# Performance work log

Hardware: AMD Instinct MI355X
Metric: run time of the kernel (lower is better)

Reference implementation:

```python
import jax, jax.numpy as jnp
import numpy as np

NF = 32      # feature channels
DG = 4       # deformable groups
K = 9        # 3x3 kernel taps


def _conv(x, w, b, stride=1):
    # x: [B,C,H,W], w: [O,I,3,3] (pad=1)
    y = jax.lax.conv_general_dilated(x, w, (stride, stride), ((1, 1), (1, 1)),
                                     dimension_numbers=('NCHW', 'OIHW', 'NCHW'))
    return y + b[None, :, None, None]


def _lrelu(x):
    return jnp.where(x >= 0, x, 0.1 * x)


def _up2(x):
    # bilinear, align_corners=False (half-pixel centers, matches torch F.interpolate)
    B, C, H, W = x.shape
    return jax.image.resize(x, (B, C, 2 * H, 2 * W), method='bilinear')


def _deform_conv(x, om, w, b):
    # Modulated deformable conv (DCNv2), stride=1, pad=1, dilation=1, 3x3.
    # x: [B,C,H,W]; om: [B,3*DG*K,H,W] = (offset_y | offset_x | mask) blocks.
    B, C, H, W = x.shape
    Cg = C // DG
    o1, o2, m = jnp.split(om, 3, axis=1)
    off_y = o1.reshape(B, DG, K, H, W)
    off_x = o2.reshape(B, DG, K, H, W)
    mask = jax.nn.sigmoid(m).reshape(B, DG, K, H, W)
    k = jnp.arange(K)
    dy = (k // 3 - 1).astype(x.dtype)            # kernel tap y displacement
    dx = (k % 3 - 1).astype(x.dtype)
    # sampling positions [B,DG,K,H,W]
    py = off_y + jnp.arange(H, dtype=x.dtype)[:, None] + dy[:, None, None]
    px = off_x + jnp.arange(W, dtype=x.dtype)[None, :] + dx[:, None, None]
    y0 = jnp.floor(py)
    x0 = jnp.floor(px)
    wy1 = py - y0
    wx1 = px - x0
    y0i = y0.astype(jnp.int32)
    x0i = x0.astype(jnp.int32)
    imgf = x.reshape(B, DG, Cg, H * W)

    def corner(yi, xi, wt):
        valid = (yi >= 0) & (yi < H) & (xi >= 0) & (xi < W)
        yc = jnp.clip(yi, 0, H - 1)
        xc = jnp.clip(xi, 0, W - 1)
        idx = (yc * W + xc).reshape(B, DG, 1, K * H * W)
        v = jnp.take_along_axis(imgf, idx, axis=3).reshape(B, DG, Cg, K, H, W)
        return v * (wt * valid)[:, :, None]

    samp = (corner(y0i, x0i, (1 - wy1) * (1 - wx1))
            + corner(y0i, x0i + 1, (1 - wy1) * wx1)
            + corner(y0i + 1, x0i, wy1 * (1 - wx1))
            + corner(y0i + 1, x0i + 1, wy1 * wx1))
    samp = samp * mask[:, :, None]                       # [B,DG,Cg,K,H,W]
    out = jnp.einsum('bgckhw,ogck->bohw', samp, w.reshape(w.shape[0], DG, Cg, K))
    return out + b[None, :, None, None]


_PARAM_SHAPES = [
    ('w1_1', (32, 64, 3, 3)), ('b1_1', (32,)),
    ('w2_1', (32, 32, 3, 3)), ('b2_1', (32,)),
    ('w3_1', (32, 32, 3, 3)), ('b3_1', (32,)),
    ('w4_1', (32, 32, 3, 3)), ('b4_1', (32,)),
    ('w6_1', (32, 32, 3, 3)), ('b6_1', (32,)),
    ('w7_1', (32, 32, 3, 3)), ('b7_1', (32,)),
    ('w1_2', (32, 64, 3, 3)), ('b1_2', (32,)),
    ('w2_2', (32, 32, 3, 3)), ('b2_2', (32,)),
    ('w3_2', (32, 64, 3, 3)), ('b3_2', (32,)),
    ('w4_2', (32, 32, 3, 3)), ('b4_2', (32,)),
    ('w_om', (108, 32, 3, 3)), ('b_om', (108,)),   # DCN_sep conv_offset_mask: 3*DG*K=108
    ('w_dcn', (32, 32, 3, 3)), ('b_dcn', (32,)),
]


def setup_inputs() -> dict:
    key = jax.random.key(0)
    ks = jax.random.split(key, len(_PARAM_SHAPES) + 2)
    B, H, W = 4, 192, 192
    d = {
        'fea1': jax.random.normal(ks[0], (B, NF, H, W), jnp.float32),
        'fea2': jax.random.normal(ks[1], (B, NF, H, W), jnp.float32),
    }
    for i, (name, shp) in enumerate(_PARAM_SHAPES):
        d[name] = jax.random.normal(ks[i + 2], shp, jnp.float32) * 0.05
    return d


def reference(fea1, fea2, w1_1, b1_1, w2_1, b2_1, w3_1, b3_1, w4_1, b4_1,
              w6_1, b6_1, w7_1, b7_1, w1_2, b1_2, w2_2, b2_2, w3_2, b3_2,
              w4_2, b4_2, w_om, b_om, w_dcn, b_dcn):
    off = _lrelu(_conv(jnp.concatenate([fea1, fea2], 1), w1_1, b1_1))
    off1 = _lrelu(_conv(off, w2_1, b2_1))
    off2 = _lrelu(_conv(off1, w3_1, b3_1, 2))   # H/2
    off2 = _lrelu(_conv(off2, w4_1, b4_1))
    off3 = _lrelu(_conv(off2, w6_1, b6_1, 2))   # H/4
    off3 = _lrelu(_conv(off3, w7_1, b7_1))
    up = _up2(off3)                              # back to H/2
    off = _lrelu(_conv(jnp.concatenate([up, off2], 1), w1_2, b1_2))
    off = _lrelu(_conv(off, w2_2, b2_2))
    up = _up2(off)                               # back to H
    off = _lrelu(_conv(jnp.concatenate([up, off1], 1), w3_2, b3_2))
    base_offset = _conv(off, w4_2, b4_2)
    om = _conv(base_offset, w_om, b_om)          # DCN_sep offset/mask head
    return _deform_conv(fea2, om, w_dcn, b_dcn)
```

## Files before the change

kernel.cpp:

```cpp
#include <hip/hip_runtime.h>
#include <math.h>


#define BDIM 256

typedef __attribute__((ext_vector_type(8))) short short8v;
typedef __attribute__((ext_vector_type(4))) float f32x4;

__device__ __forceinline__ unsigned short f2bf(float f) {
    unsigned u = __builtin_bit_cast(unsigned, f);
    u = (u + 0x7FFF + ((u >> 16) & 1)) >> 16;
    return (unsigned short)u;
}
__device__ __forceinline__ float bf2f(unsigned short h) {
    unsigned u = ((unsigned)h) << 16;
    return __builtin_bit_cast(float, u);
}

template<int NPASS, bool LRELU, int YS>
__global__ __launch_bounds__(BDIM, 2)
void convr_k(const short* __restrict__ in0, const short* __restrict__ in1,
             const short* __restrict__ wf,
             const float* __restrict__ bias,
             short* __restrict__ out, int H, int W)
{
    const int lane = threadIdx.x & 63;
    const int wid  = blockIdx.x * 4 + (threadIdx.x >> 6);
    const int segs = W >> 4;
    const int strips = (H / YS) * segs;
    const int b = wid / strips;
    int r = wid - b * strips;
    const int ys = r / segs;
    const int y0 = ys * YS;
    const int x0 = (r - ys * segs) * 16;
    const int lp = lane & 15;
    const int g  = lane >> 4;

    int colOff[3]; bool colOk[3];
#pragma unroll
    for (int tx = 0; tx < 3; ++tx) {
        const int ix = x0 + lp + tx - 1;
        colOk[tx] = (unsigned)ix < (unsigned)W;
        colOff[tx] = min(max(ix, 0), W - 1) * 32 + g * 8;
    }

    const size_t inPlane = (size_t)H * W * 32;
    const short8v zero = {};
    const short* inp0 = in0 + (size_t)b * inPlane;
    const short* inp1 = (NPASS > 1) ? in1 + (size_t)b * inPlane : nullptr;

    short8v awc[(NPASS == 1) ? 18 : 1];
    if constexpr (NPASS == 1) {
#pragma unroll
        for (int t = 0; t < 9; ++t)
#pragma unroll
            for (int h = 0; h < 2; ++h)
                awc[t * 2 + h] = *(const short8v*)(
                    wf + (((size_t)t * 2 + h) * 64 + lane) * 8);
    }

    short8v win[NPASS][3][3];

#define LOADROW(SLOT, IY) do {                                                \
        const int iy_ = (IY);                                                 \
        const bool rok_ = (unsigned)iy_ < (unsigned)H;                        \
        const int ro_ = min(max(iy_, 0), H - 1) * W;                          \
        _Pragma("unroll")                                                     \
        for (int tx = 0; tx < 3; ++tx) {                                      \
            short8v v_ = *(const short8v*)(inp0 + (size_t)ro_ * 32 + colOff[tx]); \
            win[0][SLOT][tx] = (rok_ & colOk[tx]) ? v_ : zero;                \
            if constexpr (NPASS > 1) {                                        \
                short8v w_ = *(const short8v*)(inp1 + (size_t)ro_ * 32 + colOff[tx]); \
                win[1][SLOT][tx] = (rok_ & colOk[tx]) ? w_ : zero;            \
            }                                                                 \
        }                                                                     \
    } while (0)

    LOADROW(0, y0 - 1);
    LOADROW(1, y0);

#pragma unroll
    for (int s = 0; s < YS; ++s) {
        LOADROW((s + 2) % 3, y0 + s + 1);

        f32x4 a0 = (f32x4){0.f, 0.f, 0.f, 0.f};
        f32x4 a1 = (f32x4){0.f, 0.f, 0.f, 0.f};
#pragma unroll
        for (int p = 0; p < NPASS; ++p) {
#pragma unroll
            for (int ty = 0; ty < 3; ++ty) {
#pragma unroll
                for (int tx = 0; tx < 3; ++tx) {
                    const int t = ty * 3 + tx;
                    const short8v bv = win[p][(s + ty) % 3][tx];
                    short8v av0, av1;
                    if constexpr (NPASS == 1) {
                        av0 = awc[t * 2 + 0];
                        av1 = awc[t * 2 + 1];
                    } else {
                        av0 = *(const short8v*)(
                            wf + ((((size_t)p * 9 + t) * 2 + 0) * 64 + lane) * 8);
                        av1 = *(const short8v*)(
                            wf + ((((size_t)p * 9 + t) * 2 + 1) * 64 + lane) * 8);
                    }
                    a0 = __builtin_amdgcn_mfma_f32_16x16x32_bf16(av0, bv, a0, 0, 0, 0);
                    a1 = __builtin_amdgcn_mfma_f32_16x16x32_bf16(av1, bv, a1, 0, 0, 0);
                }
            }
        }

        short* op = out + (((size_t)b * H + (y0 + s)) * W + x0 + lp) * 32;
        ushort4 st0, st1;
#pragma unroll
        for (int j = 0; j < 4; ++j) {
            float v0 = a0[j] + bias[g * 4 + j];
            float v1 = a1[j] + bias[16 + g * 4 + j];
            if (LRELU) {
                v0 = (v0 >= 0.f) ? v0 : 0.1f * v0;
                v1 = (v1 >= 0.f) ? v1 : 0.1f * v1;
            }
            ((unsigned short*)&st0)[j] = f2bf(v0);
            ((unsigned short*)&st1)[j] = f2bf(v1);
        }
        *(ushort4*)(op + g * 4) = st0;
        *(ushort4*)(op + 16 + g * 4) = st1;
    }
#undef LOADROW
}

template<int NPASS, int NHALF, int STRIDE, bool LRELU>
__global__ __launch_bounds__(BDIM, 4)
void convm_k(const short* __restrict__ in0, const short* __restrict__ in1,
             const short* __restrict__ wf,
             const float* __restrict__ bias,
             short* __restrict__ out,
             int Hin, int Win, int Hout, int Wout, int OCS)
{
    const int lane = threadIdx.x & 63;
    const int wid  = blockIdx.x * 4 + (threadIdx.x >> 6);
    const int segs = Wout >> 4;
    const int b  = wid / (Hout * segs);
    int r = wid - b * (Hout * segs);
    const int oy = r / segs;
    const int x0 = (r - oy * segs) * 16;
    const int lp = lane & 15;
    const int g  = lane >> 4;

    int rowOff[3]; bool rowOk[3];
#pragma unroll
    for (int ty = 0; ty < 3; ++ty) {
        const int iy = oy * STRIDE + ty - 1;
        rowOk[ty] = (unsigned)iy < (unsigned)Hin;
        rowOff[ty] = min(max(iy, 0), Hin - 1) * Win;
    }
    int colOff[3]; bool colOk[3];
#pragma unroll
    for (int tx = 0; tx < 3; ++tx) {
        const int ix = (x0 + lp) * STRIDE + tx - 1;
        colOk[tx] = (unsigned)ix < (unsigned)Win;
        colOff[tx] = min(max(ix, 0), Win - 1) * 32 + g * 8;
    }

    f32x4 acc[NHALF];
#pragma unroll
    for (int h = 0; h < NHALF; ++h) acc[h] = (f32x4){0.f, 0.f, 0.f, 0.f};

    const size_t inPlane = (size_t)Hin * Win * 32;
    const short8v zero = {};

#pragma unroll
    for (int pass = 0; pass < NPASS; ++pass) {
        const short* inp = (pass == 0 ? in0 : in1) + (size_t)b * inPlane;

        short8v bv[9];
#pragma unroll
        for (int t = 0; t < 9; ++t) {
            const int ty = t / 3, tx = t % 3;
            short8v v = *(const short8v*)(inp + (size_t)rowOff[ty] * 32 + colOff[tx]);
            bv[t] = (rowOk[ty] & colOk[tx]) ? v : zero;
        }
#pragma unroll
        for (int t = 0; t < 9; ++t) {
#pragma unroll
            for (int h = 0; h < NHALF; ++h) {
                short8v av = *(const short8v*)(
                    wf + ((((size_t)pass * 9 + t) * NHALF + h) * 64 + lane) * 8);
                acc[h] = __builtin_amdgcn_mfma_f32_16x16x32_bf16(av, bv[t], acc[h], 0, 0, 0);
            }
        }
    }

    short* op = out + (((size_t)b * Hout + oy) * Wout + x0 + lp) * OCS;
#pragma unroll
    for (int h = 0; h < NHALF; ++h) {
        const int co0 = h * 16 + g * 4;
        ushort4 st;
#pragma unroll
        for (int j = 0; j < 4; ++j) {
            float v = acc[h][j] + bias[co0 + j];
            if (LRELU) v = (v >= 0.f) ? v : 0.1f * v;
            ((unsigned short*)&st)[j] = f2bf(v);
        }
        *(ushort4*)(op + co0) = st;
    }
}

struct WPArgs {
    const float* src[11];
    int off[11];
    int npass[11], nhalf[11], O[11];
};

__global__ __launch_bounds__(BDIM)
void wprep_k(WPArgs a, short* __restrict__ wbase)
{
    const int z = blockIdx.z;
    const int n = a.npass[z] * 9 * a.nhalf[z] * 512;
    const int idx = blockIdx.x * BDIM + threadIdx.x;
    if (idx >= n) return;
    const int j = idx & 7;
    const int l = (idx >> 3) & 63;
    int r = idx >> 9;
    const int h = r % a.nhalf[z]; r /= a.nhalf[z];
    const int t = r % 9;
    const int pass = r / 9;
    const int I = a.npass[z] * 32;
    const int cout = h * 16 + (l & 15);
    const int cin  = pass * 32 + (l >> 4) * 8 + j;
    float v = (cout < a.O[z]) ? a.src[z][((size_t)cout * I + cin) * 9 + t] : 0.f;
    wbase[a.off[z] + idx] = (short)f2bf(v);
}

__global__ __launch_bounds__(BDIM)
void wdp_k(const float* __restrict__ w, short* __restrict__ dst)
{
    const int idx = blockIdx.x * BDIM + threadIdx.x;
    if (idx >= 9 * 2 * 64 * 8) return;
    const int j = idx & 7;
    const int l = (idx >> 3) & 63;
    const int h = (idx >> 9) & 1;
    const int k = idx >> 10;
    const int cout = h * 16 + (l & 15);
    const int cin  = (l >> 4) * 8 + j;
    dst[idx] = (short)f2bf(w[((size_t)cout * 32 + cin) * 9 + k]);
}

__global__ __launch_bounds__(BDIM)
void cvtnhwc_k(const float* __restrict__ s0, const float* __restrict__ s1,
               short* __restrict__ d0, short* __restrict__ d1, int H, int W)
{
    const float* s = blockIdx.z ? s1 : s0;
    short* d = blockIdx.z ? d1 : d0;
    const int idx = blockIdx.x * BDIM + threadIdx.x;
    if (idx >= 4 * 32 * H * W) return;
    const int c = idx & 31;
    int t = idx >> 5;
    const int x = t % W; t /= W;
    const int y = t % H;
    const int b = t / H;
    d[idx] = (short)f2bf(s[(((size_t)b * 32 + c) * H + y) * W + x]);
}

__global__ __launch_bounds__(BDIM)
void up2b_k(const short* __restrict__ in, short* __restrict__ out,
            int Hin, int Win)
{
    const int Hout = 2 * Hin, Wout = 2 * Win;
    const int idx = blockIdx.x * BDIM + threadIdx.x;
    if (idx >= 4 * Hout * Wout * 4) return;
    const int cg = idx & 3;
    int t = idx >> 2;
    const int x = t % Wout; t /= Wout;
    const int y = t % Hout;
    const int b = t / Hout;

    const float sy = (y + 0.5f) * 0.5f - 0.5f;
    const float sx = (x + 0.5f) * 0.5f - 0.5f;
    const float y0f = floorf(sy), x0f = floorf(sx);
    const float wy = sy - y0f, wx = sx - x0f;
    const int y0 = (int)y0f, x0 = (int)x0f;
    const int y0c = min(max(y0, 0), Hin - 1);
    const int y1c = min(max(y0 + 1, 0), Hin - 1);
    const int x0c = min(max(x0, 0), Win - 1);
    const int x1c = min(max(x0 + 1, 0), Win - 1);

    const short* base = in + (size_t)b * Hin * Win * 32 + cg * 8;
    short8v v00 = *(const short8v*)(base + ((size_t)y0c * Win + x0c) * 32);
    short8v v01 = *(const short8v*)(base + ((size_t)y0c * Win + x1c) * 32);
    short8v v10 = *(const short8v*)(base + ((size_t)y1c * Win + x0c) * 32);
    short8v v11 = *(const short8v*)(base + ((size_t)y1c * Win + x1c) * 32);

    short8v o;
#pragma unroll
    for (int j = 0; j < 8; ++j) {
        float f = (1.f - wy) * ((1.f - wx) * bf2f((unsigned short)v00[j]) +
                                wx * bf2f((unsigned short)v01[j]))
                + wy * ((1.f - wx) * bf2f((unsigned short)v10[j]) +
                        wx * bf2f((unsigned short)v11[j]));
        o[j] = (short)f2bf(f);
    }
    short* op = out + (size_t)b * Hout * Wout * 32 + ((size_t)y * Wout + x) * 32 + cg * 8;
    *(short8v*)op = o;
}

__global__ __launch_bounds__(BDIM, 4)
void dcnm_k(const short* __restrict__ xb,
            const short* __restrict__ bo,
            const short* __restrict__ wfo,
            const float* __restrict__ obias,
            const short* __restrict__ wfd,
            const float* __restrict__ bias,
            float* __restrict__ out, int H, int W)
{
    __shared__ unsigned short omld[4][16][112];

    const int lane = threadIdx.x & 63;
    const int wv   = threadIdx.x >> 6;
    const int wid  = blockIdx.x * 4 + wv;
    const int segs = W >> 4;
    const int b = wid / (H * segs);
    int r = wid - b * (H * segs);
    const int y = r / segs;
    const int x0 = (r - y * segs) * 16;
    const int lp = lane & 15;
    const int g  = lane >> 4;
    const int x  = x0 + lp;
    const size_t plane = (size_t)H * W;
    const short8v zero = {};

    {
        int rowOff[3]; bool rowOk[3];
#pragma unroll
        for (int ty = 0; ty < 3; ++ty) {
            const int iy = y + ty - 1;
            rowOk[ty] = (unsigned)iy < (unsigned)H;
            rowOff[ty] = min(max(iy, 0), H - 1) * W;
        }
        int colOff[3]; bool colOk[3];
#pragma unroll
        for (int tx = 0; tx < 3; ++tx) {
            const int ix = x + tx - 1;
            colOk[tx] = (unsigned)ix < (unsigned)W;
            colOff[tx] = min(max(ix, 0), W - 1) * 32 + g * 8;
        }
        const short* inp = bo + (size_t)b * plane * 32;
        short8v bv[9];
#pragma unroll
        for (int t = 0; t < 9; ++t) {
            const int ty = t / 3, tx = t % 3;
            short8v v = *(const short8v*)(inp + (size_t)rowOff[ty] * 32 + colOff[tx]);
            bv[t] = (rowOk[ty] & colOk[tx]) ? v : zero;
        }
        f32x4 acc[7];
#pragma unroll
        for (int h = 0; h < 7; ++h) acc[h] = (f32x4){0.f, 0.f, 0.f, 0.f};
#pragma unroll
        for (int t = 0; t < 9; ++t) {
#pragma unroll
            for (int h = 0; h < 7; ++h) {
                short8v av = *(const short8v*)(wfo + (((size_t)t * 7 + h) * 64 + lane) * 8);
                acc[h] = __builtin_amdgcn_mfma_f32_16x16x32_bf16(av, bv[t], acc[h], 0, 0, 0);
            }
        }
#pragma unroll
        for (int h = 0; h < 7; ++h) {
            const int co0 = h * 16 + g * 4;
            ushort4 st;
#pragma unroll
            for (int j = 0; j < 4; ++j)
                ((unsigned short*)&st)[j] = f2bf(acc[h][j] + obias[min(co0 + j, 107)]);
            *(ushort4*)&omld[wv][lp][co0] = st;
        }
    }

    f32x4 p0 = (f32x4){0.f, 0.f, 0.f, 0.f};
    f32x4 p1 = (f32x4){0.f, 0.f, 0.f, 0.f};
    const short* xbb = xb + (size_t)b * plane * 32 + g * 8;

#pragma unroll
    for (int k = 0; k < 9; ++k) {
        const float offy = bf2f(omld[wv][lp][g * 9 + k]);
        const float offx = bf2f(omld[wv][lp][36 + g * 9 + k]);
        const float ml   = bf2f(omld[wv][lp][72 + g * 9 + k]);
        const float m = 1.f / (1.f + __expf(-ml));

        const float py = offy + (float)y + (float)(k / 3 - 1);
        const float px = offx + (float)x + (float)(k % 3 - 1);
        const float y0f = floorf(py), x0f = floorf(px);
        const int y0 = (int)y0f, x0i = (int)x0f;
        const float wy1 = py - y0f, wx1 = px - x0f;
        const float wy0 = 1.f - wy1, wx0 = 1.f - wx1;

        const bool y0ok = (unsigned)y0 < (unsigned)H;
        const bool y1ok = (unsigned)(y0 + 1) < (unsigned)H;
        const bool x0ok = (unsigned)x0i < (unsigned)W;
        const bool x1ok = (unsigned)(x0i + 1) < (unsigned)W;
        const int y0c = min(max(y0, 0), H - 1);
        const int y1c = min(max(y0 + 1, 0), H - 1);
        const int x0c = min(max(x0i, 0), W - 1);
        const int x1c = min(max(x0i + 1, 0), W - 1);

        const float w00 = wy0 * wx0 * ((y0ok && x0ok) ? 1.f : 0.f) * m;
        const float w01 = wy0 * wx1 * ((y0ok && x1ok) ? 1.f : 0.f) * m;
        const float w10 = wy1 * wx0 * ((y1ok && x0ok) ? 1.f : 0.f) * m;
        const float w11 = wy1 * wx1 * ((y1ok && x1ok) ? 1.f : 0.f) * m;

        short8v v00 = *(const short8v*)(xbb + ((size_t)y0c * W + x0c) * 32);
        short8v v01 = *(const short8v*)(xbb + ((size_t)y0c * W + x1c) * 32);
        short8v v10 = *(const short8v*)(xbb + ((size_t)y1c * W + x0c) * 32);
        short8v v11 = *(const short8v*)(xbb + ((size_t)y1c * W + x1c) * 32);

        short8v bv;
#pragma unroll
        for (int j = 0; j < 8; ++j) {
            float s = w00 * bf2f((unsigned short)v00[j])
                    + w01 * bf2f((unsigned short)v01[j])
                    + w10 * bf2f((unsigned short)v10[j])
                    + w11 * bf2f((unsigned short)v11[j]);
            bv[j] = (short)f2bf(s);
        }

        short8v a0 = *(const short8v*)(wfd + (((size_t)k * 2 + 0) * 64 + lane) * 8);
        short8v a1 = *(const short8v*)(wfd + (((size_t)k * 2 + 1) * 64 + lane) * 8);
        p0 = __builtin_amdgcn_mfma_f32_16x16x32_bf16(a0, bv, p0, 0, 0, 0);
        p1 = __builtin_amdgcn_mfma_f32_16x16x32_bf16(a1, bv, p1, 0, 0, 0);
    }

    float* op = out + (size_t)b * 32 * plane + (size_t)y * W + x;
#pragma unroll
    for (int j = 0; j < 4; ++j) {
        const int co0 = g * 4 + j;
        const int co1 = 16 + g * 4 + j;
        op[(size_t)co0 * plane] = p0[j] + bias[co0];
        op[(size_t)co1 * plane] = p1[j] + bias[co1];
    }
}


extern "C" void kernel_launch(void* const* d_in, const int* in_sizes, int n_in,
                              void* d_out, int out_size, void* d_ws, size_t ws_size,
                              hipStream_t stream)
{
    const float* fea1  = (const float*)d_in[0];
    const float* fea2  = (const float*)d_in[1];
    const float* w1_1  = (const float*)d_in[2];  const float* b1_1 = (const float*)d_in[3];
    const float* w2_1  = (const float*)d_in[4];  const float* b2_1 = (const float*)d_in[5];
    const float* w3_1  = (const float*)d_in[6];  const float* b3_1 = (const float*)d_in[7];
    const float* w4_1  = (const float*)d_in[8];  const float* b4_1 = (const float*)d_in[9];
    const float* w6_1  = (const float*)d_in[10]; const float* b6_1 = (const float*)d_in[11];
    const float* w7_1  = (const float*)d_in[12]; const float* b7_1 = (const float*)d_in[13];
    const float* w1_2  = (const float*)d_in[14]; const float* b1_2 = (const float*)d_in[15];
    const float* w2_2  = (const float*)d_in[16]; const float* b2_2 = (const float*)d_in[17];
    const float* w3_2  = (const float*)d_in[18]; const float* b3_2 = (const float*)d_in[19];
    const float* w4_2  = (const float*)d_in[20]; const float* b4_2 = (const float*)d_in[21];
    const float* w_om  = (const float*)d_in[22]; const float* b_om = (const float*)d_in[23];
    const float* w_dcn = (const float*)d_in[24]; const float* b_dcn= (const float*)d_in[25];

    const int H = 192, W = 192;
    char* ws = (char*)d_ws;

    short* fea1b = (short*)(ws + 0);
    short* fea2b = (short*)(ws + 9437184);
    short* bufA  = (short*)(ws + 18874368);
    short* bufB  = (short*)(ws + 28311552);
    short* bufC  = (short*)(ws + 0);
    short* bufD  = (short*)(ws + 2359296);
    short* bufE  = (short*)(ws + 4718592);
    short* bufF  = (short*)(ws + 5308416);
    short* bufG  = (short*)(ws + 5898240);
    short* bufH  = (short*)(ws + 0);
    short* bufI  = (short*)(ws + 4718592);
    short* bufJ  = (short*)(ws + 37748736);
    short* bufK  = (short*)(ws + 18874368);
    short* bufL  = (short*)(ws + 0);
    short* wfrag = (short*)(ws + 70778880);
    short* wfdcn = (short*)(ws + 71083008);

    const int WOFF[11] = {0, 18432, 27648, 36864, 46080, 55296,
                          64512, 82944, 92160, 110592, 119808};

    dim3 blk(BDIM, 1, 1);

    {
        WPArgs a;
        const float* srcs[11] = {w1_1, w2_1, w3_1, w4_1, w6_1, w7_1,
                                 w1_2, w2_2, w3_2, w4_2, w_om};
        const int NP[11] = {2,1,1,1,1,1,2,1,2,1,1};
        const int NH[11] = {2,2,2,2,2,2,2,2,2,2,7};
        const int Os[11] = {32,32,32,32,32,32,32,32,32,32,108};
        for (int i = 0; i < 11; ++i) {
            a.src[i] = srcs[i]; a.off[i] = WOFF[i];
            a.npass[i] = NP[i]; a.nhalf[i] = NH[i]; a.O[i] = Os[i];
        }
        wprep_k<<<dim3(126, 1, 11), blk, 0, stream>>>(a, wfrag);
        cvtnhwc_k<<<dim3(18432, 1, 2), blk, 0, stream>>>(fea1, fea2, fea1b, fea2b, H, W);
        wdp_k<<<dim3(36), blk, 0, stream>>>(w_dcn, wfdcn);
    }

    convr_k<2,true,4><<<dim3(576), blk, 0, stream>>>(
        fea1b, fea2b, wfrag + WOFF[0], b1_1, bufA, 192, 192);
    convr_k<1,true,4><<<dim3(576), blk, 0, stream>>>(
        bufA, nullptr, wfrag + WOFF[1], b2_1, bufB, 192, 192);
    convm_k<1,2,2,true><<<dim3(576), blk, 0, stream>>>(
        bufB, nullptr, wfrag + WOFF[2], b3_1, bufC, 192,192,96,96, 32);
    convm_k<1,2,1,true><<<dim3(576), blk, 0, stream>>>(
        bufC, nullptr, wfrag + WOFF[3], b4_1, bufD, 96,96,96,96, 32);
    convm_k<1,2,2,true><<<dim3(144), blk, 0, stream>>>(
        bufD, nullptr, wfrag + WOFF[4], b6_1, bufE, 96,96,48,48, 32);
    convm_k<1,2,1,true><<<dim3(144), blk, 0, stream>>>(
        bufE, nullptr, wfrag + WOFF[5], b7_1, bufF, 48,48,48,48, 32);
    up2b_k<<<dim3(576), blk, 0, stream>>>(bufF, bufG, 48, 48);
    convm_k<2,2,1,true><<<dim3(576), blk, 0, stream>>>(
        bufG, bufD, wfrag + WOFF[6], b1_2, bufH, 96,96,96,96, 32);
    convm_k<1,2,1,true><<<dim3(576), blk, 0, stream>>>(
        bufH, nullptr, wfrag + WOFF[7], b2_2, bufI, 96,96,96,96, 32);
    up2b_k<<<dim3(2304), blk, 0, stream>>>(bufI, bufJ, 96, 96);
    convr_k<2,true,4><<<dim3(576), blk, 0, stream>>>(
        bufJ, bufB, wfrag + WOFF[8], b3_2, bufK, 192, 192);
    convr_k<1,false,4><<<dim3(576), blk, 0, stream>>>(
        bufK, nullptr, wfrag + WOFF[9], b4_2, bufL, 192, 192);
    dcnm_k<<<dim3(2304), blk, 0, stream>>>(
        fea2b, bufL, wfrag + WOFF[10], b_om, wfdcn, b_dcn, (float*)d_out, H, W);
}
```

Measured before the change: 313.3 us.

## Batch DCN gather loads, shrink conv row strips, retune launch bounds

The deformable-conv kernel now computes all bilinear weights and gather indices first, then issues the twelve corner loads for three taps together before the blend-and-MFMA step. This exposes more memory-level parallelism for the gathers. The LDS row for the offset/mask tile is padded from 112 to 116, presumably to cut bank conflicts. The full-resolution convs switch from 4-row to 2-row strips with twice as many blocks, and launch-bound occupancy hints change (convr 2→3, dcnm 4→3). The trade-offs are higher register pressure from the batched loads and less vertical reuse in the smaller conv strips.

```diff
diff --git a/kernel.cpp b/kernel.cpp
--- a/kernel.cpp
+++ b/kernel.cpp
@@ -18,7 +18,7 @@
 }
 
 template<int NPASS, bool LRELU, int YS>
-__global__ __launch_bounds__(BDIM, 2)
+__global__ __launch_bounds__(BDIM, 3)
 void convr_k(const short* __restrict__ in0, const short* __restrict__ in1,
              const short* __restrict__ wf,
              const float* __restrict__ bias,
@@ -303,7 +303,7 @@
     *(short8v*)op = o;
 }
 
-__global__ __launch_bounds__(BDIM, 4)
+__global__ __launch_bounds__(BDIM, 3)
 void dcnm_k(const short* __restrict__ xb,
             const short* __restrict__ bo,
             const short* __restrict__ wfo,
@@ -312,7 +312,7 @@
             const float* __restrict__ bias,
             float* __restrict__ out, int H, int W)
 {
-    __shared__ unsigned short omld[4][16][112];
+    __shared__ unsigned short omld[4][16][116];
 
     const int lane = threadIdx.x & 63;
     const int wv   = threadIdx.x >> 6;
@@ -373,10 +373,8 @@
         }
     }
 
-    f32x4 p0 = (f32x4){0.f, 0.f, 0.f, 0.f};
-    f32x4 p1 = (f32x4){0.f, 0.f, 0.f, 0.f};
-    const short* xbb = xb + (size_t)b * plane * 32 + g * 8;
-
+    float wts[9][4];
+    int   ia[9][4];
 #pragma unroll
     for (int k = 0; k < 9; ++k) {
         const float offy = bf2f(omld[wv][lp][g * 9 + k]);
@@ -400,30 +398,47 @@
         const int x0c = min(max(x0i, 0), W - 1);
         const int x1c = min(max(x0i + 1, 0), W - 1);
 
-        const float w00 = wy0 * wx0 * ((y0ok && x0ok) ? 1.f : 0.f) * m;
-        const float w01 = wy0 * wx1 * ((y0ok && x1ok) ? 1.f : 0.f) * m;
-        const float w10 = wy1 * wx0 * ((y1ok && x0ok) ? 1.f : 0.f) * m;
-        const float w11 = wy1 * wx1 * ((y1ok && x1ok) ? 1.f : 0.f) * m;
-
-        short8v v00 = *(const short8v*)(xbb + ((size_t)y0c * W + x0c) * 32);
-        short8v v01 = *(const short8v*)(xbb + ((size_t)y0c * W + x1c) * 32);
-        short8v v10 = *(const short8v*)(xbb + ((size_t)y1c * W + x0c) * 32);
-        short8v v11 = *(const short8v*)(xbb + ((size_t)y1c * W + x1c) * 32);
-
-        short8v bv;
-#pragma unroll
-        for (int j = 0; j < 8; ++j) {
-            float s = w00 * bf2f((unsigned short)v00[j])
-                    + w01 * bf2f((unsigned short)v01[j])
-                    + w10 * bf2f((unsigned short)v10[j])
-                    + w11 * bf2f((unsigned short)v11[j]);
-            bv[j] = (short)f2bf(s);
-        }
-
-        short8v a0 = *(const short8v*)(wfd + (((size_t)k * 2 + 0) * 64 + lane) * 8);
-        short8v a1 = *(const short8v*)(wfd + (((size_t)k * 2 + 1) * 64 + lane) * 8);
-        p0 = __builtin_amdgcn_mfma_f32_16x16x32_bf16(a0, bv, p0, 0, 0, 0);
-        p1 = __builtin_amdgcn_mfma_f32_16x16x32_bf16(a1, bv, p1, 0, 0, 0);
+        wts[k][0] = wy0 * wx0 * ((y0ok && x0ok) ? 1.f : 0.f) * m;
+        wts[k][1] = wy0 * wx1 * ((y0ok && x1ok) ? 1.f : 0.f) * m;
+        wts[k][2] = wy1 * wx0 * ((y1ok && x0ok) ? 1.f : 0.f) * m;
+        wts[k][3] = wy1 * wx1 * ((y1ok && x1ok) ? 1.f : 0.f) * m;
+        ia[k][0] = y0c * W + x0c;
+        ia[k][1] = y0c * W + x1c;
+        ia[k][2] = y1c * W + x0c;
+        ia[k][3] = y1c * W + x1c;
+    }
+
+    f32x4 p0 = (f32x4){0.f, 0.f, 0.f, 0.f};
+    f32x4 p1 = (f32x4){0.f, 0.f, 0.f, 0.f};
+    const short* xbb = xb + (size_t)b * plane * 32 + g * 8;
+
+#pragma unroll
+    for (int gi = 0; gi < 3; ++gi) {
+        short8v cd[12];
+#pragma unroll
+        for (int t = 0; t < 3; ++t) {
+            const int k = gi * 3 + t;
+#pragma unroll
+            for (int c = 0; c < 4; ++c)
+                cd[t * 4 + c] = *(const short8v*)(xbb + (size_t)ia[k][c] * 32);
+        }
+#pragma unroll
+        for (int t = 0; t < 3; ++t) {
+            const int k = gi * 3 + t;
+            short8v bv;
+#pragma unroll
+            for (int j = 0; j < 8; ++j) {
+                float s = wts[k][0] * bf2f((unsigned short)cd[t * 4 + 0][j])
+                        + wts[k][1] * bf2f((unsigned short)cd[t * 4 + 1][j])
+                        + wts[k][2] * bf2f((unsigned short)cd[t * 4 + 2][j])
+                        + wts[k][3] * bf2f((unsigned short)cd[t * 4 + 3][j]);
+                bv[j] = (short)f2bf(s);
+            }
+            short8v a0 = *(const short8v*)(wfd + (((size_t)k * 2 + 0) * 64 + lane) * 8);
+            short8v a1 = *(const short8v*)(wfd + (((size_t)k * 2 + 1) * 64 + lane) * 8);
+            p0 = __builtin_amdgcn_mfma_f32_16x16x32_bf16(a0, bv, p0, 0, 0, 0);
+            p1 = __builtin_amdgcn_mfma_f32_16x16x32_bf16(a1, bv, p1, 0, 0, 0);
+        }
     }
 
     float* op = out + (size_t)b * 32 * plane + (size_t)y * W + x;
@@ -497,9 +512,9 @@
         wdp_k<<<dim3(36), blk, 0, stream>>>(w_dcn, wfdcn);
     }
 
-    convr_k<2,true,4><<<dim3(576), blk, 0, stream>>>(
+    convr_k<2,true,2><<<dim3(1152), blk, 0, stream>>>(
         fea1b, fea2b, wfrag + WOFF[0], b1_1, bufA, 192, 192);
-    convr_k<1,true,4><<<dim3(576), blk, 0, stream>>>(
+    convr_k<1,true,2><<<dim3(1152), blk, 0, stream>>>(
         bufA, nullptr, wfrag + WOFF[1], b2_1, bufB, 192, 192);
     convm_k<1,2,2,true><<<dim3(576), blk, 0, stream>>>(
         bufB, nullptr, wfrag + WOFF[2], b3_1, bufC, 192,192,96,96, 32);
@@ -515,9 +530,9 @@
     convm_k<1,2,1,true><<<dim3(576), blk, 0, stream>>>(
         bufH, nullptr, wfrag + WOFF[7], b2_2, bufI, 96,96,96,96, 32);
     up2b_k<<<dim3(2304), blk, 0, stream>>>(bufI, bufJ, 96, 96);
-    convr_k<2,true,4><<<dim3(576), blk, 0, stream>>>(
+    convr_k<2,true,2><<<dim3(1152), blk, 0, stream>>>(
         bufJ, bufB, wfrag + WOFF[8], b3_2, bufK, 192, 192);
-    convr_k<1,false,4><<<dim3(576), blk, 0, stream>>>(
+    convr_k<1,false,2><<<dim3(1152), blk, 0, stream>>>(
         bufK, nullptr, wfrag + WOFF[9], b4_2, bufL, 192, 192);
     dcnm_k<<<dim3(2304), blk, 0, stream>>>(
         fea2b, bufL, wfrag + WOFF[10], b_om, wfdcn, b_dcn, (float*)d_out, H, W);
```

New measurement: 311.2 us. No clear change (-0.7%).

## Split convr output channels across waves and shrink row strips for parallelism

Applied to the files above, without the earlier changes.

Each full-resolution conv wave now computes only one 16-channel half of the output (chosen by wave parity), with strips shortened from four rows to two, so the grid grows fourfold. This lowers per-wave register use, which allows higher launch-bound occupancy, and gives more waves to hide latency. The cost is that each input window is loaded twice, once per half, and rows are reloaded more often with shorter strips. The DCN shared-memory row is also padded from 112 to 116 to reduce bank conflicts.

```diff
diff --git a/kernel.cpp b/kernel.cpp
--- a/kernel.cpp
+++ b/kernel.cpp
@@ -18,7 +18,7 @@
 }
 
 template<int NPASS, bool LRELU, int YS>
-__global__ __launch_bounds__(BDIM, 2)
+__global__ __launch_bounds__(BDIM, NPASS == 1 ? 4 : 3)
 void convr_k(const short* __restrict__ in0, const short* __restrict__ in1,
              const short* __restrict__ wf,
              const float* __restrict__ bias,
@@ -26,10 +26,12 @@
 {
     const int lane = threadIdx.x & 63;
     const int wid  = blockIdx.x * 4 + (threadIdx.x >> 6);
+    const int hh   = wid & 1;
+    const int sw   = wid >> 1;
     const int segs = W >> 4;
     const int strips = (H / YS) * segs;
-    const int b = wid / strips;
-    int r = wid - b * strips;
+    const int b = sw / strips;
+    int r = sw - b * strips;
     const int ys = r / segs;
     const int y0 = ys * YS;
     const int x0 = (r - ys * segs) * 16;
@@ -49,15 +51,10 @@
     const short* inp0 = in0 + (size_t)b * inPlane;
     const short* inp1 = (NPASS > 1) ? in1 + (size_t)b * inPlane : nullptr;
 
-    short8v awc[(NPASS == 1) ? 18 : 1];
-    if constexpr (NPASS == 1) {
-#pragma unroll
-        for (int t = 0; t < 9; ++t)
-#pragma unroll
-            for (int h = 0; h < 2; ++h)
-                awc[t * 2 + h] = *(const short8v*)(
-                    wf + (((size_t)t * 2 + h) * 64 + lane) * 8);
-    }
+    short8v awc[9];
+#pragma unroll
+    for (int t = 0; t < 9; ++t)
+        awc[t] = *(const short8v*)(wf + (((size_t)t * 2 + hh) * 64 + lane) * 8);
 
     short8v win[NPASS][3][3];
 
@@ -84,7 +81,6 @@
         LOADROW((s + 2) % 3, y0 + s + 1);
 
         f32x4 a0 = (f32x4){0.f, 0.f, 0.f, 0.f};
-        f32x4 a1 = (f32x4){0.f, 0.f, 0.f, 0.f};
 #pragma unroll
         for (int p = 0; p < NPASS; ++p) {
 #pragma unroll
@@ -93,37 +89,27 @@
                 for (int tx = 0; tx < 3; ++tx) {
                     const int t = ty * 3 + tx;
                     const short8v bv = win[p][(s + ty) % 3][tx];
-                    short8v av0, av1;
-                    if constexpr (NPASS == 1) {
-                        av0 = awc[t * 2 + 0];
-                        av1 = awc[t * 2 + 1];
+                    short8v av;
+                    if (p == 0) {
+                        av = awc[t];
                     } else {
-                        av0 = *(const short8v*)(
-                            wf + ((((size_t)p * 9 + t) * 2 + 0) * 64 + lane) * 8);
-                        av1 = *(const short8v*)(
-                            wf + ((((size_t)p * 9 + t) * 2 + 1) * 64 + lane) * 8);
+                        av = *(const short8v*)(
+                            wf + ((((size_t)9 + t) * 2 + hh) * 64 + lane) * 8);
                     }
-                    a0 = __builtin_amdgcn_mfma_f32_16x16x32_bf16(av0, bv, a0, 0, 0, 0);
-                    a1 = __builtin_amdgcn_mfma_f32_16x16x32_bf16(av1, bv, a1, 0, 0, 0);
+                    a0 = __builtin_amdgcn_mfma_f32_16x16x32_bf16(av, bv, a0, 0, 0, 0);
                 }
             }
         }
 
         short* op = out + (((size_t)b * H + (y0 + s)) * W + x0 + lp) * 32;
-        ushort4 st0, st1;
+        ushort4 st0;
 #pragma unroll
         for (int j = 0; j < 4; ++j) {
-            float v0 = a0[j] + bias[g * 4 + j];
-            float v1 = a1[j] + bias[16 + g * 4 + j];
-            if (LRELU) {
-                v0 = (v0 >= 0.f) ? v0 : 0.1f * v0;
-                v1 = (v1 >= 0.f) ? v1 : 0.1f * v1;
-            }
+            float v0 = a0[j] + bias[hh * 16 + g * 4 + j];
+            if (LRELU) v0 = (v0 >= 0.f) ? v0 : 0.1f * v0;
             ((unsigned short*)&st0)[j] = f2bf(v0);
-            ((unsigned short*)&st1)[j] = f2bf(v1);
-        }
-        *(ushort4*)(op + g * 4) = st0;
-        *(ushort4*)(op + 16 + g * 4) = st1;
+        }
+        *(ushort4*)(op + hh * 16 + g * 4) = st0;
     }
 #undef LOADROW
 }
@@ -312,7 +298,7 @@
             const float* __restrict__ bias,
             float* __restrict__ out, int H, int W)
 {
-    __shared__ unsigned short omld[4][16][112];
+    __shared__ unsigned short omld[4][16][116];
 
     const int lane = threadIdx.x & 63;
     const int wv   = threadIdx.x >> 6;
@@ -497,9 +483,9 @@
         wdp_k<<<dim3(36), blk, 0, stream>>>(w_dcn, wfdcn);
     }
 
-    convr_k<2,true,4><<<dim3(576), blk, 0, stream>>>(
+    convr_k<2,true,2><<<dim3(2304), blk, 0, stream>>>(
         fea1b, fea2b, wfrag + WOFF[0], b1_1, bufA, 192, 192);
-    convr_k<1,true,4><<<dim3(576), blk, 0, stream>>>(
+    convr_k<1,true,2><<<dim3(2304), blk, 0, stream>>>(
         bufA, nullptr, wfrag + WOFF[1], b2_1, bufB, 192, 192);
     convm_k<1,2,2,true><<<dim3(576), blk, 0, stream>>>(
         bufB, nullptr, wfrag + WOFF[2], b3_1, bufC, 192,192,96,96, 32);
@@ -515,9 +501,9 @@
     convm_k<1,2,1,true><<<dim3(576), blk, 0, stream>>>(
         bufH, nullptr, wfrag + WOFF[7], b2_2, bufI, 96,96,96,96, 32);
     up2b_k<<<dim3(2304), blk, 0, stream>>>(bufI, bufJ, 96, 96);
-    convr_k<2,true,4><<<dim3(576), blk, 0, stream>>>(
+    convr_k<2,true,2><<<dim3(2304), blk, 0, stream>>>(
         bufJ, bufB, wfrag + WOFF[8], b3_2, bufK, 192, 192);
-    convr_k<1,false,4><<<dim3(576), blk, 0, stream>>>(
+    convr_k<1,false,2><<<dim3(2304), blk, 0, stream>>>(
         bufK, nullptr, wfrag + WOFF[9], b4_2, bufL, 192, 192);
     dcnm_k<<<dim3(2304), blk, 0, stream>>>(
         fea2b, bufL, wfrag + WOFF[10], b_om, wfdcn, b_dcn, (float*)d_out, H, W);
```

New measurement: 316.5 us. About the same (+1.0%).
